# Optimization experiments

Measured on AMD Instinct MI355X. Metric: run time of the kernel, lower is better.

## Reference

```python
import jax, jax.numpy as jnp
import numpy as np

N_PER_G = 18
GRAPHS = 4096
N = GRAPHS * N_PER_G            # 73728 nodes
E = GRAPHS * N_PER_G * (N_PER_G - 1)  # 1253376 edges (fully connected per graph)
F_IN = 1536                     # sfreq * timestep
EPS = 1e-5
SLOPE = 0.01


def _lrelu(v):
    return jnp.where(v >= 0, v, SLOPE * v)


def setup_inputs() -> dict:
    key = jax.random.key(0)
    ks = jax.random.split(key, 32)
    # node features
    x = jax.random.normal(ks[0], (N, F_IN), dtype=jnp.float32)
    # fully-connected edges within each 18-node graph
    src, dst = np.meshgrid(np.arange(N_PER_G), np.arange(N_PER_G), indexing='ij')
    m = src != dst
    src, dst = src[m], dst[m]                      # [306]
    offs = (np.arange(GRAPHS) * N_PER_G)[:, None]
    row = (offs + src[None, :]).reshape(-1)
    col = (offs + dst[None, :]).reshape(-1)
    edge_index = jnp.asarray(np.stack([row, col]), dtype=jnp.int32)  # [2,E]
    edge_weight = jax.random.uniform(ks[1], (E,), dtype=jnp.float32)
    batch = jnp.asarray(np.arange(N) // N_PER_G, dtype=jnp.int32)

    def lin(k, fi, fo):
        kw, kb = jax.random.split(k)
        s = 1.0 / np.sqrt(fi)
        W = jax.random.uniform(kw, (fi, fo), jnp.float32, -s, s)
        b = jax.random.uniform(kb, (fo,), jnp.float32, -s, s)
        return W, b

    def bn(k, f):
        k1, k2 = jax.random.split(k)
        g = jnp.ones((f,), jnp.float32)
        be = jnp.zeros((f,), jnp.float32)
        rm = jax.random.normal(k1, (f,), jnp.float32) * 0.1
        rv = jax.random.uniform(k2, (f,), jnp.float32) + 0.5
        return g, be, rm, rv

    W1, b1 = lin(ks[2], F_IN, 32)
    W2, b2 = lin(ks[3], 32, 64)
    W3, b3 = lin(ks[4], 64, 128)
    g1, be1, rm1, rv1 = bn(ks[5], 32)
    g2, be2, rm2, rv2 = bn(ks[6], 64)
    g3, be3, rm3, rv3 = bn(ks[7], 128)
    fW1, fb1 = lin(ks[8], 128, 64)
    fW2, fb2 = lin(ks[9], 64, 32)
    fW3, fb3 = lin(ks[10], 32, 16)
    fW4, fb4 = lin(ks[11], 16, 1)

    return dict(x=x, edge_index=edge_index, edge_weight=edge_weight, batch=batch,
                W1=W1, b1=b1, g1=g1, be1=be1, rm1=rm1, rv1=rv1,
                W2=W2, b2=b2, g2=g2, be2=be2, rm2=rm2, rv2=rv2,
                W3=W3, b3=b3, g3=g3, be3=be3, rm3=rm3, rv3=rv3,
                fW1=fW1, fb1=fb1, fW2=fW2, fb2=fb2,
                fW3=fW3, fb3=fb3, fW4=fW4, fb4=fb4)


def _gcn_norm(edge_index, edge_weight):
    # add self loops (weight 1), symmetric normalization (PyG GCNConv, improved=False)
    row = jnp.concatenate([edge_index[0], jnp.arange(N, dtype=edge_index.dtype)])
    col = jnp.concatenate([edge_index[1], jnp.arange(N, dtype=edge_index.dtype)])
    w = jnp.concatenate([edge_weight, jnp.ones((N,), edge_weight.dtype)])
    deg = jax.ops.segment_sum(w, col, num_segments=N)
    dinv = jnp.where(deg > 0, jax.lax.rsqrt(jnp.maximum(deg, 1e-30)), 0.0)
    norm = dinv[row] * w * dinv[col]
    return row, col, norm


def _gcn(x, W, b, row, col, norm):
    h = x @ W                                       # [N, Fout]
    out = jax.ops.segment_sum(norm[:, None] * h[row], col, num_segments=N)
    return out + b


def _bn(h, g, be, rm, rv):
    return (h - rm) * jax.lax.rsqrt(rv + EPS) * g + be


def reference(x, edge_index, edge_weight, batch,
              W1, b1, g1, be1, rm1, rv1,
              W2, b2, g2, be2, rm2, rv2,
              W3, b3, g3, be3, rm3, rv3,
              fW1, fb1, fW2, fb2, fW3, fb3, fW4, fb4):
    row, col, norm = _gcn_norm(edge_index, edge_weight)
    h = _lrelu(_bn(_gcn(x, W1, b1, row, col, norm), g1, be1, rm1, rv1))
    h = _lrelu(_bn(_gcn(h, W2, b2, row, col, norm), g2, be2, rm2, rv2))
    h = _lrelu(_bn(_gcn(h, W3, b3, row, col, norm), g3, be3, rm3, rv3))
    # global mean pool over graphs
    sums = jax.ops.segment_sum(h, batch, num_segments=GRAPHS)
    cnt = jax.ops.segment_sum(jnp.ones((N,), h.dtype), batch, num_segments=GRAPHS)
    h = sums / jnp.maximum(cnt, 1.0)[:, None]       # [G,128]
    # MLP head (dropout = identity in eval)
    h = _lrelu(h @ fW1 + fb1)
    h = _lrelu(h @ fW2 + fb2)
    h = _lrelu(h @ fW3 + fb3)
    h = h @ fW4 + fb4
    return h.squeeze(-1)                            # [G]
```

## Files before the change

kernel.cpp:

```cpp
#include <hip/hip_runtime.h>
#include <stdint.h>

#define GRAPHS 4096
#define NPG 18
#define EPERG 306
#define FIN 1536
#define BN_EPS 1e-5f
#define SLOPE 0.01f

using short8  = __attribute__((ext_vector_type(8))) short;
using ushort8 = __attribute__((ext_vector_type(8))) unsigned short;
using f32x4   = __attribute__((ext_vector_type(4))) float;

__device__ __forceinline__ unsigned short f2bf(float f) {
  unsigned u = __builtin_bit_cast(unsigned, f);
  u += 0x7fffu + ((u >> 16) & 1u);
  return (unsigned short)(u >> 16);
}

__global__ void prep_kernel(const float* __restrict__ W1,
    const float* __restrict__ b1, const float* __restrict__ g1,
    const float* __restrict__ be1, const float* __restrict__ rm1, const float* __restrict__ rv1,
    const float* __restrict__ b2, const float* __restrict__ g2,
    const float* __restrict__ be2, const float* __restrict__ rm2, const float* __restrict__ rv2,
    const float* __restrict__ b3, const float* __restrict__ g3,
    const float* __restrict__ be3, const float* __restrict__ rm3, const float* __restrict__ rv3,
    unsigned short* __restrict__ w1frag, float* __restrict__ ab) {
  const int tid = threadIdx.x;
  if (blockIdx.x < 24) {
    int slot = blockIdx.x * 256 + tid;
    int L  = slot & 63;
    int nt = (slot >> 6) & 1;
    int ks = slot >> 7;
    int n  = nt * 16 + (L & 15);
    int kb = ks * 32 + ((L >> 4) << 3);
    ushort8 v;
#pragma unroll
    for (int j = 0; j < 8; ++j) v[j] = f2bf(W1[(kb + j) * 32 + n]);
    *((ushort8*)w1frag + slot) = v;
  } else {
    if (tid < 32) {
      float a = g1[tid] * rsqrtf(rv1[tid] + BN_EPS);
      ab[tid] = a; ab[32 + tid] = (b1[tid] - rm1[tid]) * a + be1[tid];
    }
    if (tid < 64) {
      float a = g2[tid] * rsqrtf(rv2[tid] + BN_EPS);
      ab[64 + tid] = a; ab[128 + tid] = (b2[tid] - rm2[tid]) * a + be2[tid];
    }
    if (tid < 128) {
      float a = g3[tid] * rsqrtf(rv3[tid] + BN_EPS);
      ab[192 + tid] = a; ab[320 + tid] = (b3[tid] - rm3[tid]) * a + be3[tid];
    }
  }
}

__global__ __launch_bounds__(256, 4) void gcn_main(
    const float* __restrict__ x, const float* __restrict__ ew,
    const float* __restrict__ W2, const float* __restrict__ W3,
    const float* __restrict__ fW1, const float* __restrict__ fb1,
    const float* __restrict__ fW2, const float* __restrict__ fb2,
    const float* __restrict__ fW3, const float* __restrict__ fb3,
    const float* __restrict__ fW4, const float* __restrict__ fb4,
    const unsigned short* __restrict__ w1frag, const float* __restrict__ ab,
    float* __restrict__ out) {
  const int g    = blockIdx.x;
  const int tid  = threadIdx.x;
  const int lane = tid & 63;
  const int wv   = tid >> 6;

  __shared__ float ew_s[EPERG];
  __shared__ float dinv_s[NPG];
  __shared__ float An[NPG][NPG + 1];
  __shared__ short xA[32][136];
  __shared__ float Pb[NPG][129];
  __shared__ float Hb[NPG][129];
  __shared__ float pooled[128];
  __shared__ float m1[64];
  __shared__ float m2[32];
  __shared__ float m3[16];

  for (int i = tid; i < EPERG; i += 256) ew_s[i] = ew[g * EPERG + i];
  for (int i = tid; i < 14 * 68; i += 256) {
    int r = 18 + i / 68, c = i % 68;
    ((int*)&xA[r][0])[c] = 0;
  }
  __syncthreads();

  if (tid < NPG) {
    float deg = 1.0f;
#pragma unroll
    for (int j = 0; j < 17; ++j) {
      int s = j + (j >= tid);
      deg += ew_s[s * 17 + (tid - (tid > s ? 1 : 0))];
    }
    dinv_s[tid] = rsqrtf(deg);
  }
  __syncthreads();

  for (int o = tid; o < NPG * NPG; o += 256) {
    int d = o / NPG, s = o - d * NPG;
    float v;
    if (d == s) v = dinv_s[d] * dinv_s[d];
    else        v = dinv_s[s] * ew_s[s * 17 + (d - (d > s ? 1 : 0))] * dinv_s[d];
    An[d][s] = v;
  }

  const int Mt = wv & 1, Nt = wv >> 1;
  const int arow  = Mt * 16 + (lane & 15);
  const int akoff = (lane >> 4) << 3;
  f32x4 acc = {0.f, 0.f, 0.f, 0.f};
  const float4* __restrict__ x4 = (const float4*)x + (size_t)g * 18 * 384;

  for (int c = 0; c < 12; ++c) {
    const int k0d4 = c * 32;
    for (int idx = tid; idx < 576; idx += 256) {
      int r = idx >> 5, c4 = idx & 31;
      float4 v = x4[r * 384 + k0d4 + c4];
      ushort4 b;
      b.x = f2bf(v.x); b.y = f2bf(v.y); b.z = f2bf(v.z); b.w = f2bf(v.w);
      *(ushort4*)(&xA[r][c4 * 4]) = b;
    }
    __syncthreads();
#pragma unroll
    for (int kk = 0; kk < 4; ++kk) {
      short8 af = *(const short8*)(&xA[arow][kk * 32 + akoff]);
      short8 bf = *(const short8*)(w1frag + (size_t)(((c * 4 + kk) * 2 + Nt) * 64 + lane) * 8);
      acc = __builtin_amdgcn_mfma_f32_16x16x32_bf16(af, bf, acc, 0, 0, 0);
    }
    __syncthreads();
  }

  {
    int ccol  = Nt * 16 + (lane & 15);
    int rbase = Mt * 16 + ((lane >> 4) << 2);
#pragma unroll
    for (int q = 0; q < 4; ++q) {
      int rr = rbase + q;
      if (rr < NPG) Pb[rr][ccol] = acc[q];
    }
  }
  __syncthreads();

  for (int o = tid; o < NPG * 32; o += 256) {
    int d = o >> 5, cc = o & 31;
    float s = 0.f;
#pragma unroll
    for (int ss = 0; ss < NPG; ++ss) s = fmaf(An[d][ss], Pb[ss][cc], s);
    float v = fmaf(s, ab[cc], ab[32 + cc]);
    Hb[d][cc] = v >= 0.f ? v : SLOPE * v;
  }
  __syncthreads();

  for (int o = tid; o < NPG * 64; o += 256) {
    int r = o >> 6, cc = o & 63;
    float s = 0.f;
#pragma unroll
    for (int k = 0; k < 32; ++k) s = fmaf(Hb[r][k], W2[k * 64 + cc], s);
    Pb[r][cc] = s;
  }
  __syncthreads();
  for (int o = tid; o < NPG * 64; o += 256) {
    int d = o >> 6, cc = o & 63;
    float s = 0.f;
#pragma unroll
    for (int ss = 0; ss < NPG; ++ss) s = fmaf(An[d][ss], Pb[ss][cc], s);
    float v = fmaf(s, ab[64 + cc], ab[128 + cc]);
    Hb[d][cc] = v >= 0.f ? v : SLOPE * v;
  }
  __syncthreads();

  for (int o = tid; o < NPG * 128; o += 256) {
    int r = o >> 7, cc = o & 127;
    float s = 0.f;
#pragma unroll
    for (int k = 0; k < 64; ++k) s = fmaf(Hb[r][k], W3[k * 128 + cc], s);
    Pb[r][cc] = s;
  }
  __syncthreads();
  for (int o = tid; o < NPG * 128; o += 256) {
    int d = o >> 7, cc = o & 127;
    float s = 0.f;
#pragma unroll
    for (int ss = 0; ss < NPG; ++ss) s = fmaf(An[d][ss], Pb[ss][cc], s);
    float v = fmaf(s, ab[192 + cc], ab[320 + cc]);
    Hb[d][cc] = v >= 0.f ? v : SLOPE * v;
  }
  __syncthreads();

  if (tid < 128) {
    float s = 0.f;
#pragma unroll
    for (int d = 0; d < NPG; ++d) s += Hb[d][tid];
    pooled[tid] = s * (1.0f / 18.0f);
  }
  __syncthreads();
  if (tid < 64) {
    float s = fb1[tid];
#pragma unroll 8
    for (int k = 0; k < 128; ++k) s = fmaf(pooled[k], fW1[k * 64 + tid], s);
    m1[tid] = s >= 0.f ? s : SLOPE * s;
  }
  __syncthreads();
  if (tid < 32) {
    float s = fb2[tid];
#pragma unroll
    for (int k = 0; k < 64; ++k) s = fmaf(m1[k], fW2[k * 32 + tid], s);
    m2[tid] = s >= 0.f ? s : SLOPE * s;
  }
  __syncthreads();
  if (tid < 16) {
    float s = fb3[tid];
#pragma unroll
    for (int k = 0; k < 32; ++k) s = fmaf(m2[k], fW3[k * 16 + tid], s);
    m3[tid] = s >= 0.f ? s : SLOPE * s;
  }
  __syncthreads();
  if (tid == 0) {
    float s = fb4[0];
#pragma unroll
    for (int k = 0; k < 16; ++k) s = fmaf(m3[k], fW4[k], s);
    out[g] = s;
  }
}

extern "C" void kernel_launch(void* const* d_in, const int* in_sizes, int n_in,
                              void* d_out, int out_size, void* d_ws, size_t ws_size,
                              hipStream_t stream) {
  const float* x   = (const float*)d_in[0];
  const float* ew  = (const float*)d_in[2];
  const float* W1  = (const float*)d_in[4];
  const float* b1  = (const float*)d_in[5];
  const float* g1  = (const float*)d_in[6];
  const float* be1 = (const float*)d_in[7];
  const float* rm1 = (const float*)d_in[8];
  const float* rv1 = (const float*)d_in[9];
  const float* W2  = (const float*)d_in[10];
  const float* b2  = (const float*)d_in[11];
  const float* g2  = (const float*)d_in[12];
  const float* be2 = (const float*)d_in[13];
  const float* rm2 = (const float*)d_in[14];
  const float* rv2 = (const float*)d_in[15];
  const float* W3  = (const float*)d_in[16];
  const float* b3  = (const float*)d_in[17];
  const float* g3  = (const float*)d_in[18];
  const float* be3 = (const float*)d_in[19];
  const float* rm3 = (const float*)d_in[20];
  const float* rv3 = (const float*)d_in[21];
  const float* fW1 = (const float*)d_in[22];
  const float* fb1 = (const float*)d_in[23];
  const float* fW2 = (const float*)d_in[24];
  const float* fb2 = (const float*)d_in[25];
  const float* fW3 = (const float*)d_in[26];
  const float* fb3 = (const float*)d_in[27];
  const float* fW4 = (const float*)d_in[28];
  const float* fb4 = (const float*)d_in[29];

  unsigned short* w1frag = (unsigned short*)d_ws;
  float* ab = (float*)((char*)d_ws + 98304);

  prep_kernel<<<25, 256, 0, stream>>>(W1, b1, g1, be1, rm1, rv1,
                                      b2, g2, be2, rm2, rv2,
                                      b3, g3, be3, rm3, rv3, w1frag, ab);
  gcn_main<<<GRAPHS, 256, 0, stream>>>(x, ew, W2, W3, fW1, fb1, fW2, fb2,
                                       fW3, fb3, fW4, fb4, w1frag, ab,
                                       (float*)d_out);
}
```

Baseline: 730.5 us.

## Split layer-1 GEMM into a flat MFMA kernel and reorder GCN aggregation

The per-graph layer-1 GEMM, which staged x through shared memory with a barrier per chunk, becomes a separate streaming kernel. It reads x rows directly into registers, converts them to bf16 and issues MFMAs over 16-row tiles, writing the projected features to a workspace buffer. The remaining kernel reads those features and reorders layers 2 and 3 so aggregation runs before the weight multiply, which shrinks aggregation width. The dense layers use pre-transposed weights with float4 dot products. This costs an extra launch and a global round trip for the intermediate buffer, in exchange for removing shared-memory staging and barriers from the memory-bound part.

```diff
diff --git a/kernel.cpp b/kernel.cpp
--- a/kernel.cpp
+++ b/kernel.cpp
@@ -25,7 +25,10 @@
     const float* __restrict__ be2, const float* __restrict__ rm2, const float* __restrict__ rv2,
     const float* __restrict__ b3, const float* __restrict__ g3,
     const float* __restrict__ be3, const float* __restrict__ rm3, const float* __restrict__ rv3,
-    unsigned short* __restrict__ w1frag, float* __restrict__ ab) {
+    const float* __restrict__ W2, const float* __restrict__ W3,
+    const float* __restrict__ fW1,
+    unsigned short* __restrict__ w1frag, float* __restrict__ ab,
+    float* __restrict__ W2t, float* __restrict__ W3t, float* __restrict__ fW1t) {
   const int tid = threadIdx.x;
   if (blockIdx.x < 24) {
     int slot = blockIdx.x * 256 + tid;
@@ -38,7 +41,7 @@
 #pragma unroll
     for (int j = 0; j < 8; ++j) v[j] = f2bf(W1[(kb + j) * 32 + n]);
     *((ushort8*)w1frag + slot) = v;
-  } else {
+  } else if (blockIdx.x == 24) {
     if (tid < 32) {
       float a = g1[tid] * rsqrtf(rv1[tid] + BN_EPS);
       ab[tid] = a; ab[32 + tid] = (b1[tid] - rm1[tid]) * a + be1[tid];
@@ -51,39 +54,85 @@
       float a = g3[tid] * rsqrtf(rv3[tid] + BN_EPS);
       ab[192 + tid] = a; ab[320 + tid] = (b3[tid] - rm3[tid]) * a + be3[tid];
     }
-  }
-}
-
-__global__ __launch_bounds__(256, 4) void gcn_main(
-    const float* __restrict__ x, const float* __restrict__ ew,
-    const float* __restrict__ W2, const float* __restrict__ W3,
-    const float* __restrict__ fW1, const float* __restrict__ fb1,
+  } else if (blockIdx.x == 25) {
+    for (int i = tid; i < 64 * 32; i += 256) {
+      int cc = i >> 5, k = i & 31;
+      W2t[i] = W2[k * 64 + cc];
+    }
+  } else if (blockIdx.x == 26) {
+    for (int i = tid; i < 128 * 64; i += 256) {
+      int cc = i >> 6, k = i & 63;
+      W3t[i] = W3[k * 128 + cc];
+    }
+  } else {
+    for (int i = tid; i < 64 * 128; i += 256) {
+      int cc = i >> 7, k = i & 127;
+      fW1t[i] = fW1[k * 64 + cc];
+    }
+  }
+}
+
+__global__ __launch_bounds__(128, 4) void l1_gemm(
+    const float* __restrict__ x, const unsigned short* __restrict__ w1frag,
+    float* __restrict__ p1) {
+  const int lane = threadIdx.x & 63;
+  const int wv   = threadIdx.x >> 6;
+  const int mt   = blockIdx.x * 2 + wv;
+  const int row  = mt * 16 + (lane & 15);
+  const float* __restrict__ xr = x + (size_t)row * FIN + ((lane >> 4) << 3);
+  const short8* __restrict__ wf = (const short8*)w1frag + lane;
+
+  f32x4 acc0 = {0.f, 0.f, 0.f, 0.f};
+  f32x4 acc1 = {0.f, 0.f, 0.f, 0.f};
+
+#pragma unroll 4
+  for (int ks = 0; ks < 48; ++ks) {
+    float4 a0 = *(const float4*)(xr + ks * 32);
+    float4 a1 = *(const float4*)(xr + ks * 32 + 4);
+    short8 af;
+    af[0] = (short)f2bf(a0.x); af[1] = (short)f2bf(a0.y);
+    af[2] = (short)f2bf(a0.z); af[3] = (short)f2bf(a0.w);
+    af[4] = (short)f2bf(a1.x); af[5] = (short)f2bf(a1.y);
+    af[6] = (short)f2bf(a1.z); af[7] = (short)f2bf(a1.w);
+    short8 b0 = wf[(ks * 2 + 0) * 64];
+    short8 b1 = wf[(ks * 2 + 1) * 64];
+    acc0 = __builtin_amdgcn_mfma_f32_16x16x32_bf16(af, b0, acc0, 0, 0, 0);
+    acc1 = __builtin_amdgcn_mfma_f32_16x16x32_bf16(af, b1, acc1, 0, 0, 0);
+  }
+
+  const int crow = mt * 16 + ((lane >> 4) << 2);
+  const int ccol = lane & 15;
+  float* p = p1 + (size_t)crow * 32 + ccol;
+#pragma unroll
+  for (int q = 0; q < 4; ++q) {
+    p[q * 32]      = acc0[q];
+    p[q * 32 + 16] = acc1[q];
+  }
+}
+
+__global__ __launch_bounds__(256, 4) void gcn_rest(
+    const float* __restrict__ ew, const float* __restrict__ p1,
+    const float* __restrict__ W2t, const float* __restrict__ W3t,
+    const float* __restrict__ fW1t, const float* __restrict__ fb1,
     const float* __restrict__ fW2, const float* __restrict__ fb2,
     const float* __restrict__ fW3, const float* __restrict__ fb3,
     const float* __restrict__ fW4, const float* __restrict__ fb4,
-    const unsigned short* __restrict__ w1frag, const float* __restrict__ ab,
-    float* __restrict__ out) {
-  const int g    = blockIdx.x;
-  const int tid  = threadIdx.x;
-  const int lane = tid & 63;
-  const int wv   = tid >> 6;
+    const float* __restrict__ ab, float* __restrict__ out) {
+  const int g   = blockIdx.x;
+  const int tid = threadIdx.x;
 
   __shared__ float ew_s[EPERG];
   __shared__ float dinv_s[NPG];
   __shared__ float An[NPG][NPG + 1];
-  __shared__ short xA[32][136];
-  __shared__ float Pb[NPG][129];
-  __shared__ float Hb[NPG][129];
-  __shared__ float pooled[128];
+  __shared__ __align__(16) float Pb[NPG][132];
+  __shared__ __align__(16) float Hb[NPG][132];
+  __shared__ __align__(16) float pooled[128];
   __shared__ float m1[64];
   __shared__ float m2[32];
   __shared__ float m3[16];
 
   for (int i = tid; i < EPERG; i += 256) ew_s[i] = ew[g * EPERG + i];
-  for (int i = tid; i < 14 * 68; i += 256) {
-    int r = 18 + i / 68, c = i % 68;
-    ((int*)&xA[r][0])[c] = 0;
-  }
+  for (int i = tid; i < NPG * 32; i += 256) Pb[i >> 5][i & 31] = p1[g * 576 + i];
   __syncthreads();
 
   if (tid < NPG) {
@@ -104,41 +153,6 @@
     else        v = dinv_s[s] * ew_s[s * 17 + (d - (d > s ? 1 : 0))] * dinv_s[d];
     An[d][s] = v;
   }
-
-  const int Mt = wv & 1, Nt = wv >> 1;
-  const int arow  = Mt * 16 + (lane & 15);
-  const int akoff = (lane >> 4) << 3;
-  f32x4 acc = {0.f, 0.f, 0.f, 0.f};
-  const float4* __restrict__ x4 = (const float4*)x + (size_t)g * 18 * 384;
-
-  for (int c = 0; c < 12; ++c) {
-    const int k0d4 = c * 32;
-    for (int idx = tid; idx < 576; idx += 256) {
-      int r = idx >> 5, c4 = idx & 31;
-      float4 v = x4[r * 384 + k0d4 + c4];
-      ushort4 b;
-      b.x = f2bf(v.x); b.y = f2bf(v.y); b.z = f2bf(v.z); b.w = f2bf(v.w);
-      *(ushort4*)(&xA[r][c4 * 4]) = b;
-    }
-    __syncthreads();
-#pragma unroll
-    for (int kk = 0; kk < 4; ++kk) {
-      short8 af = *(const short8*)(&xA[arow][kk * 32 + akoff]);
-      short8 bf = *(const short8*)(w1frag + (size_t)(((c * 4 + kk) * 2 + Nt) * 64 + lane) * 8);
-      acc = __builtin_amdgcn_mfma_f32_16x16x32_bf16(af, bf, acc, 0, 0, 0);
-    }
-    __syncthreads();
-  }
-
-  {
-    int ccol  = Nt * 16 + (lane & 15);
-    int rbase = Mt * 16 + ((lane >> 4) << 2);
-#pragma unroll
-    for (int q = 0; q < 4; ++q) {
-      int rr = rbase + q;
-      if (rr < NPG) Pb[rr][ccol] = acc[q];
-    }
-  }
   __syncthreads();
 
   for (int o = tid; o < NPG * 32; o += 256) {
@@ -151,39 +165,53 @@
   }
   __syncthreads();
 
+  for (int o = tid; o < NPG * 32; o += 256) {
+    int d = o >> 5, cc = o & 31;
+    float s = 0.f;
+#pragma unroll
+    for (int ss = 0; ss < NPG; ++ss) s = fmaf(An[d][ss], Hb[ss][cc], s);
+    Pb[d][cc] = s;
+  }
+  __syncthreads();
+
   for (int o = tid; o < NPG * 64; o += 256) {
     int r = o >> 6, cc = o & 63;
-    float s = 0.f;
-#pragma unroll
-    for (int k = 0; k < 32; ++k) s = fmaf(Hb[r][k], W2[k * 64 + cc], s);
-    Pb[r][cc] = s;
-  }
-  __syncthreads();
+    const float4* gp = (const float4*)(&Pb[r][0]);
+    const float4* wp = (const float4*)(W2t + cc * 32);
+    float s = 0.f;
+#pragma unroll
+    for (int k4 = 0; k4 < 8; ++k4) {
+      float4 a = gp[k4], b = wp[k4];
+      s = fmaf(a.x, b.x, s); s = fmaf(a.y, b.y, s);
+      s = fmaf(a.z, b.z, s); s = fmaf(a.w, b.w, s);
+    }
+    float v = fmaf(s, ab[64 + cc], ab[128 + cc]);
+    Hb[r][cc] = v >= 0.f ? v : SLOPE * v;
+  }
+  __syncthreads();
+
   for (int o = tid; o < NPG * 64; o += 256) {
     int d = o >> 6, cc = o & 63;
     float s = 0.f;
 #pragma unroll
-    for (int ss = 0; ss < NPG; ++ss) s = fmaf(An[d][ss], Pb[ss][cc], s);
-    float v = fmaf(s, ab[64 + cc], ab[128 + cc]);
-    Hb[d][cc] = v >= 0.f ? v : SLOPE * v;
+    for (int ss = 0; ss < NPG; ++ss) s = fmaf(An[d][ss], Hb[ss][cc], s);
+    Pb[d][cc] = s;
   }
   __syncthreads();
 
   for (int o = tid; o < NPG * 128; o += 256) {
     int r = o >> 7, cc = o & 127;
-    float s = 0.f;
-#pragma unroll
-    for (int k = 0; k < 64; ++k) s = fmaf(Hb[r][k], W3[k * 128 + cc], s);
-    Pb[r][cc] = s;
-  }
-  __syncthreads();
-  for (int o = tid; o < NPG * 128; o += 256) {
-    int d = o >> 7, cc = o & 127;
-    float s = 0.f;
-#pragma unroll
-    for (int ss = 0; ss < NPG; ++ss) s = fmaf(An[d][ss], Pb[ss][cc], s);
+    const float4* gp = (const float4*)(&Pb[r][0]);
+    const float4* wp = (const float4*)(W3t + cc * 64);
+    float s = 0.f;
+#pragma unroll
+    for (int k4 = 0; k4 < 16; ++k4) {
+      float4 a = gp[k4], b = wp[k4];
+      s = fmaf(a.x, b.x, s); s = fmaf(a.y, b.y, s);
+      s = fmaf(a.z, b.z, s); s = fmaf(a.w, b.w, s);
+    }
     float v = fmaf(s, ab[192 + cc], ab[320 + cc]);
-    Hb[d][cc] = v >= 0.f ? v : SLOPE * v;
+    Hb[r][cc] = v >= 0.f ? v : SLOPE * v;
   }
   __syncthreads();
 
@@ -195,9 +223,15 @@
   }
   __syncthreads();
   if (tid < 64) {
+    const float4* pp = (const float4*)pooled;
+    const float4* wp = (const float4*)(fW1t + tid * 128);
     float s = fb1[tid];
-#pragma unroll 8
-    for (int k = 0; k < 128; ++k) s = fmaf(pooled[k], fW1[k * 64 + tid], s);
+#pragma unroll
+    for (int k4 = 0; k4 < 32; ++k4) {
+      float4 a = pp[k4], b = wp[k4];
+      s = fmaf(a.x, b.x, s); s = fmaf(a.y, b.y, s);
+      s = fmaf(a.z, b.z, s); s = fmaf(a.w, b.w, s);
+    }
     m1[tid] = s >= 0.f ? s : SLOPE * s;
   }
   __syncthreads();
@@ -256,12 +290,18 @@
   const float* fb4 = (const float*)d_in[29];
 
   unsigned short* w1frag = (unsigned short*)d_ws;
-  float* ab = (float*)((char*)d_ws + 98304);
-
-  prep_kernel<<<25, 256, 0, stream>>>(W1, b1, g1, be1, rm1, rv1,
+  float* ab   = (float*)((char*)d_ws + 98304);
+  float* W2t  = (float*)((char*)d_ws + 100352);
+  float* W3t  = (float*)((char*)d_ws + 108544);
+  float* fW1t = (float*)((char*)d_ws + 141312);
+  float* p1   = (float*)((char*)d_ws + 174080);
+
+  prep_kernel<<<28, 256, 0, stream>>>(W1, b1, g1, be1, rm1, rv1,
                                       b2, g2, be2, rm2, rv2,
-                                      b3, g3, be3, rm3, rv3, w1frag, ab);
-  gcn_main<<<GRAPHS, 256, 0, stream>>>(x, ew, W2, W3, fW1, fb1, fW2, fb2,
-                                       fW3, fb3, fW4, fb4, w1frag, ab,
-                                       (float*)d_out);
-}
+                                      b3, g3, be3, rm3, rv3,
+                                      W2, W3, fW1,
+                                      w1frag, ab, W2t, W3t, fW1t);
+  l1_gemm<<<2304, 128, 0, stream>>>(x, w1frag, p1);
+  gcn_rest<<<GRAPHS, 256, 0, stream>>>(ew, p1, W2t, W3t, fW1t, fb1, fW2, fb2,
+                                       fW3, fb3, fW4, fb4, ab, (float*)d_out);
+}
```

Result: slower. 747.0 us (+2.3%).

## Batch eight graphs per block with register-fed MFMA and per-wave GCN layers

Applied to the files above, without the earlier changes.

Each block now handles eight graphs. The first-layer projection reads x directly from global memory into bf16 MFMA fragments, with no LDS staging or per-chunk barriers. Later layers and the MLP head run per wave with only waitcnt fences, and aggregation is reordered to come before the small dense projections. The grid shrinks to 512 blocks, which lowers parallelism and raises register pressure (large wc arrays).

```diff
diff --git a/kernel.cpp b/kernel.cpp
--- a/kernel.cpp
+++ b/kernel.cpp
@@ -7,6 +7,9 @@
 #define FIN 1536
 #define BN_EPS 1e-5f
 #define SLOPE 0.01f
+#define GPB 8
+#define RPB 144
+#define NTILE 9
 
 using short8  = __attribute__((ext_vector_type(8))) short;
 using ushort8 = __attribute__((ext_vector_type(8))) unsigned short;
@@ -16,6 +19,19 @@
   unsigned u = __builtin_bit_cast(unsigned, f);
   u += 0x7fffu + ((u >> 16) & 1u);
   return (unsigned short)(u >> 16);
+}
+
+__device__ __forceinline__ short8 pack_bf16(const float4& a0, const float4& a1) {
+  short8 af;
+  af[0] = (short)f2bf(a0.x); af[1] = (short)f2bf(a0.y);
+  af[2] = (short)f2bf(a0.z); af[3] = (short)f2bf(a0.w);
+  af[4] = (short)f2bf(a1.x); af[5] = (short)f2bf(a1.y);
+  af[6] = (short)f2bf(a1.z); af[7] = (short)f2bf(a1.w);
+  return af;
+}
+
+__device__ __forceinline__ void wave_fence() {
+  asm volatile("s_waitcnt lgkmcnt(0)" ::: "memory");
 }
 
 __global__ void prep_kernel(const float* __restrict__ W1,
@@ -54,172 +70,196 @@
   }
 }
 
-__global__ __launch_bounds__(256, 4) void gcn_main(
+__global__ __launch_bounds__(256, 2) void gcn_fused(
     const float* __restrict__ x, const float* __restrict__ ew,
+    const unsigned short* __restrict__ w1frag, const float* __restrict__ ab,
     const float* __restrict__ W2, const float* __restrict__ W3,
     const float* __restrict__ fW1, const float* __restrict__ fb1,
     const float* __restrict__ fW2, const float* __restrict__ fb2,
     const float* __restrict__ fW3, const float* __restrict__ fb3,
     const float* __restrict__ fW4, const float* __restrict__ fb4,
-    const unsigned short* __restrict__ w1frag, const float* __restrict__ ab,
     float* __restrict__ out) {
-  const int g    = blockIdx.x;
+  const int bid  = blockIdx.x;
   const int tid  = threadIdx.x;
   const int lane = tid & 63;
   const int wv   = tid >> 6;
 
-  __shared__ float ew_s[EPERG];
-  __shared__ float dinv_s[NPG];
-  __shared__ float An[NPG][NPG + 1];
-  __shared__ short xA[32][136];
-  __shared__ float Pb[NPG][129];
-  __shared__ float Hb[NPG][129];
-  __shared__ float pooled[128];
-  __shared__ float m1[64];
-  __shared__ float m2[32];
-  __shared__ float m3[16];
-
-  for (int i = tid; i < EPERG; i += 256) ew_s[i] = ew[g * EPERG + i];
-  for (int i = tid; i < 14 * 68; i += 256) {
-    int r = 18 + i / 68, c = i % 68;
-    ((int*)&xA[r][0])[c] = 0;
+  __shared__ __align__(16) float P1[RPB][36];
+  __shared__ float ew_s[GPB * EPERG];
+  __shared__ float dinv_s[GPB][NPG];
+  __shared__ float An_s[GPB][NPG][19];
+  __shared__ __align__(16) float BufA[4][NPG][68];
+  __shared__ __align__(16) float BufB[4][NPG][68];
+
+  for (int i = tid; i < GPB * EPERG; i += 256)
+    ew_s[i] = ew[(size_t)bid * (GPB * EPERG) + i];
+
+  const int arow = lane & 15;
+  const int akg  = lane >> 4;
+  const short8* __restrict__ wf = (const short8*)w1frag + lane;
+  const float* __restrict__ xg = x + (size_t)bid * RPB * FIN;
+
+  for (int t = wv; t < NTILE; t += 4) {
+    f32x4 acc0 = {0.f, 0.f, 0.f, 0.f};
+    f32x4 acc1 = {0.f, 0.f, 0.f, 0.f};
+    const float* __restrict__ xr = xg + (size_t)(t * 16 + arow) * FIN + (akg << 3);
+#pragma unroll 4
+    for (int ks = 0; ks < 48; ++ks) {
+      float4 a0 = *(const float4*)(xr + ks * 32);
+      float4 a1 = *(const float4*)(xr + ks * 32 + 4);
+      short8 af = pack_bf16(a0, a1);
+      acc0 = __builtin_amdgcn_mfma_f32_16x16x32_bf16(af, wf[(ks * 2 + 0) * 64], acc0, 0, 0, 0);
+      acc1 = __builtin_amdgcn_mfma_f32_16x16x32_bf16(af, wf[(ks * 2 + 1) * 64], acc1, 0, 0, 0);
+    }
+    const int crow = t * 16 + (akg << 2);
+#pragma unroll
+    for (int q = 0; q < 4; ++q) {
+      P1[crow + q][arow]      = acc0[q];
+      P1[crow + q][arow + 16] = acc1[q];
+    }
   }
   __syncthreads();
 
-  if (tid < NPG) {
+  if (tid < GPB * NPG) {
+    int j = tid / NPG, d = tid - j * NPG;
+    const float* e = ew_s + j * EPERG;
     float deg = 1.0f;
 #pragma unroll
-    for (int j = 0; j < 17; ++j) {
-      int s = j + (j >= tid);
-      deg += ew_s[s * 17 + (tid - (tid > s ? 1 : 0))];
-    }
-    dinv_s[tid] = rsqrtf(deg);
+    for (int k = 0; k < 17; ++k) {
+      int s = k + (k >= d);
+      deg += e[s * 17 + (d - (d > s ? 1 : 0))];
+    }
+    dinv_s[j][d] = rsqrtf(deg);
   }
   __syncthreads();
 
-  for (int o = tid; o < NPG * NPG; o += 256) {
-    int d = o / NPG, s = o - d * NPG;
+  for (int o = tid; o < GPB * NPG * NPG; o += 256) {
+    int j = o / (NPG * NPG), rm = o - j * (NPG * NPG);
+    int d = rm / NPG, s = rm - d * NPG;
     float v;
-    if (d == s) v = dinv_s[d] * dinv_s[d];
-    else        v = dinv_s[s] * ew_s[s * 17 + (d - (d > s ? 1 : 0))] * dinv_s[d];
-    An[d][s] = v;
-  }
-
-  const int Mt = wv & 1, Nt = wv >> 1;
-  const int arow  = Mt * 16 + (lane & 15);
-  const int akoff = (lane >> 4) << 3;
-  f32x4 acc = {0.f, 0.f, 0.f, 0.f};
-  const float4* __restrict__ x4 = (const float4*)x + (size_t)g * 18 * 384;
-
-  for (int c = 0; c < 12; ++c) {
-    const int k0d4 = c * 32;
-    for (int idx = tid; idx < 576; idx += 256) {
-      int r = idx >> 5, c4 = idx & 31;
-      float4 v = x4[r * 384 + k0d4 + c4];
-      ushort4 b;
-      b.x = f2bf(v.x); b.y = f2bf(v.y); b.z = f2bf(v.z); b.w = f2bf(v.w);
-      *(ushort4*)(&xA[r][c4 * 4]) = b;
-    }
-    __syncthreads();
-#pragma unroll
-    for (int kk = 0; kk < 4; ++kk) {
-      short8 af = *(const short8*)(&xA[arow][kk * 32 + akoff]);
-      short8 bf = *(const short8*)(w1frag + (size_t)(((c * 4 + kk) * 2 + Nt) * 64 + lane) * 8);
-      acc = __builtin_amdgcn_mfma_f32_16x16x32_bf16(af, bf, acc, 0, 0, 0);
-    }
-    __syncthreads();
-  }
-
-  {
-    int ccol  = Nt * 16 + (lane & 15);
-    int rbase = Mt * 16 + ((lane >> 4) << 2);
-#pragma unroll
-    for (int q = 0; q < 4; ++q) {
-      int rr = rbase + q;
-      if (rr < NPG) Pb[rr][ccol] = acc[q];
-    }
+    if (d == s) v = dinv_s[j][d] * dinv_s[j][d];
+    else        v = dinv_s[j][s] * ew_s[j * EPERG + s * 17 + (d - (d > s ? 1 : 0))] * dinv_s[j][d];
+    An_s[j][d][s] = v;
   }
   __syncthreads();
 
-  for (int o = tid; o < NPG * 32; o += 256) {
-    int d = o >> 5, cc = o & 31;
-    float s = 0.f;
-#pragma unroll
-    for (int ss = 0; ss < NPG; ++ss) s = fmaf(An[d][ss], Pb[ss][cc], s);
-    float v = fmaf(s, ab[cc], ab[32 + cc]);
-    Hb[d][cc] = v >= 0.f ? v : SLOPE * v;
-  }
-  __syncthreads();
-
-  for (int o = tid; o < NPG * 64; o += 256) {
-    int r = o >> 6, cc = o & 63;
-    float s = 0.f;
-#pragma unroll
-    for (int k = 0; k < 32; ++k) s = fmaf(Hb[r][k], W2[k * 64 + cc], s);
-    Pb[r][cc] = s;
-  }
-  __syncthreads();
-  for (int o = tid; o < NPG * 64; o += 256) {
-    int d = o >> 6, cc = o & 63;
-    float s = 0.f;
-#pragma unroll
-    for (int ss = 0; ss < NPG; ++ss) s = fmaf(An[d][ss], Pb[ss][cc], s);
-    float v = fmaf(s, ab[64 + cc], ab[128 + cc]);
-    Hb[d][cc] = v >= 0.f ? v : SLOPE * v;
-  }
-  __syncthreads();
-
-  for (int o = tid; o < NPG * 128; o += 256) {
-    int r = o >> 7, cc = o & 127;
-    float s = 0.f;
-#pragma unroll
-    for (int k = 0; k < 64; ++k) s = fmaf(Hb[r][k], W3[k * 128 + cc], s);
-    Pb[r][cc] = s;
-  }
-  __syncthreads();
-  for (int o = tid; o < NPG * 128; o += 256) {
-    int d = o >> 7, cc = o & 127;
-    float s = 0.f;
-#pragma unroll
-    for (int ss = 0; ss < NPG; ++ss) s = fmaf(An[d][ss], Pb[ss][cc], s);
-    float v = fmaf(s, ab[192 + cc], ab[320 + cc]);
-    Hb[d][cc] = v >= 0.f ? v : SLOPE * v;
-  }
-  __syncthreads();
-
-  if (tid < 128) {
-    float s = 0.f;
-#pragma unroll
-    for (int d = 0; d < NPG; ++d) s += Hb[d][tid];
-    pooled[tid] = s * (1.0f / 18.0f);
-  }
-  __syncthreads();
-  if (tid < 64) {
-    float s = fb1[tid];
-#pragma unroll 8
-    for (int k = 0; k < 128; ++k) s = fmaf(pooled[k], fW1[k * 64 + tid], s);
-    m1[tid] = s >= 0.f ? s : SLOPE * s;
-  }
-  __syncthreads();
-  if (tid < 32) {
-    float s = fb2[tid];
-#pragma unroll
-    for (int k = 0; k < 64; ++k) s = fmaf(m1[k], fW2[k * 32 + tid], s);
-    m2[tid] = s >= 0.f ? s : SLOPE * s;
-  }
-  __syncthreads();
-  if (tid < 16) {
-    float s = fb3[tid];
-#pragma unroll
-    for (int k = 0; k < 32; ++k) s = fmaf(m2[k], fW3[k * 16 + tid], s);
-    m3[tid] = s >= 0.f ? s : SLOPE * s;
-  }
-  __syncthreads();
-  if (tid == 0) {
-    float s = fb4[0];
-#pragma unroll
-    for (int k = 0; k < 16; ++k) s = fmaf(m3[k], fW4[k], s);
-    out[g] = s;
+  float (*A_)[68] = BufA[wv];
+  float (*B_)[68] = BufB[wv];
+
+#pragma unroll 1
+  for (int jj = 0; jj < 2; ++jj) {
+    const int j = wv + (jj << 2);
+    const float (*An)[19] = An_s[j];
+    const float* P1g = &P1[j * NPG][0];
+
+    for (int o4 = lane; o4 < 144; o4 += 64) {
+      int d = o4 >> 3, cb = (o4 & 7) << 2;
+      f32x4 s = {0.f, 0.f, 0.f, 0.f};
+#pragma unroll
+      for (int ss = 0; ss < NPG; ++ss) {
+        float a = An[d][ss];
+        f32x4 p = *(const f32x4*)(P1g + ss * 36 + cb);
+        s[0] = fmaf(a, p[0], s[0]); s[1] = fmaf(a, p[1], s[1]);
+        s[2] = fmaf(a, p[2], s[2]); s[3] = fmaf(a, p[3], s[3]);
+      }
+      f32x4 al = *(const f32x4*)(ab + cb), be = *(const f32x4*)(ab + 32 + cb);
+#pragma unroll
+      for (int q = 0; q < 4; ++q) {
+        float v = fmaf(s[q], al[q], be[q]);
+        s[q] = v >= 0.f ? v : SLOPE * v;
+      }
+      *(f32x4*)&A_[d][cb] = s;
+    }
+    wave_fence();
+
+    for (int o4 = lane; o4 < 144; o4 += 64) {
+      int d = o4 >> 3, cb = (o4 & 7) << 2;
+      f32x4 s = {0.f, 0.f, 0.f, 0.f};
+#pragma unroll
+      for (int ss = 0; ss < NPG; ++ss) {
+        float a = An[d][ss];
+        f32x4 p = *(const f32x4*)&A_[ss][cb];
+        s[0] = fmaf(a, p[0], s[0]); s[1] = fmaf(a, p[1], s[1]);
+        s[2] = fmaf(a, p[2], s[2]); s[3] = fmaf(a, p[3], s[3]);
+      }
+      *(f32x4*)&B_[d][cb] = s;
+    }
+    wave_fence();
+
+    {
+      float wc[32];
+#pragma unroll
+      for (int k = 0; k < 32; ++k) wc[k] = W2[k * 64 + lane];
+      const float al = ab[64 + lane], be = ab[128 + lane];
+      for (int r2 = 0; r2 < NPG; ++r2) {
+        float s = 0.f;
+#pragma unroll
+        for (int k4 = 0; k4 < 8; ++k4) {
+          f32x4 g = *(const f32x4*)&B_[r2][k4 * 4];
+          s = fmaf(g[0], wc[k4 * 4 + 0], s); s = fmaf(g[1], wc[k4 * 4 + 1], s);
+          s = fmaf(g[2], wc[k4 * 4 + 2], s); s = fmaf(g[3], wc[k4 * 4 + 3], s);
+        }
+        float v = fmaf(s, al, be);
+        A_[r2][lane] = v >= 0.f ? v : SLOPE * v;
+      }
+    }
+    wave_fence();
+
+    for (int o4 = lane; o4 < 288; o4 += 64) {
+      int d = o4 >> 4, cb = (o4 & 15) << 2;
+      f32x4 s = {0.f, 0.f, 0.f, 0.f};
+#pragma unroll
+      for (int ss = 0; ss < NPG; ++ss) {
+        float a = An[d][ss];
+        f32x4 p = *(const f32x4*)&A_[ss][cb];
+        s[0] = fmaf(a, p[0], s[0]); s[1] = fmaf(a, p[1], s[1]);
+        s[2] = fmaf(a, p[2], s[2]); s[3] = fmaf(a, p[3], s[3]);
+      }
+      *(f32x4*)&B_[d][cb] = s;
+    }
+    wave_fence();
+
+    float pool0 = 0.f, pool1 = 0.f;
+#pragma unroll
+    for (int h = 0; h < 2; ++h) {
+      const int cc = (h << 6) + lane;
+      float wc[64];
+#pragma unroll
+      for (int k = 0; k < 64; ++k) wc[k] = W3[k * 128 + cc];
+      const float al = ab[192 + cc], be = ab[320 + cc];
+      float pr = 0.f;
+      for (int r3 = 0; r3 < NPG; ++r3) {
+        float s = 0.f;
+#pragma unroll
+        for (int k4 = 0; k4 < 16; ++k4) {
+          f32x4 g = *(const f32x4*)&B_[r3][k4 * 4];
+          s = fmaf(g[0], wc[k4 * 4 + 0], s); s = fmaf(g[1], wc[k4 * 4 + 1], s);
+          s = fmaf(g[2], wc[k4 * 4 + 2], s); s = fmaf(g[3], wc[k4 * 4 + 3], s);
+        }
+        float v = fmaf(s, al, be);
+        pr += (v >= 0.f ? v : SLOPE * v);
+      }
+      if (h == 0) pool0 = pr * (1.0f / 18.0f); else pool1 = pr * (1.0f / 18.0f);
+    }
+
+    float s1 = fb1[lane];
+#pragma unroll
+    for (int k = 0; k < 64; ++k) s1 = fmaf(__shfl(pool0, k), fW1[k * 64 + lane], s1);
+#pragma unroll
+    for (int k = 0; k < 64; ++k) s1 = fmaf(__shfl(pool1, k), fW1[(64 + k) * 64 + lane], s1);
+    s1 = s1 >= 0.f ? s1 : SLOPE * s1;
+    float s2 = fb2[lane & 31];
+#pragma unroll
+    for (int k = 0; k < 64; ++k) s2 = fmaf(__shfl(s1, k), fW2[k * 32 + (lane & 31)], s2);
+    s2 = s2 >= 0.f ? s2 : SLOPE * s2;
+    float s3 = fb3[lane & 15];
+#pragma unroll
+    for (int k = 0; k < 32; ++k) s3 = fmaf(__shfl(s2, k), fW3[k * 16 + (lane & 15)], s3);
+    s3 = s3 >= 0.f ? s3 : SLOPE * s3;
+    float s4 = fb4[0];
+#pragma unroll
+    for (int k = 0; k < 16; ++k) s4 = fmaf(__shfl(s3, k), fW4[k], s4);
+    if (lane == 0) out[(bid << 3) + j] = s4;
   }
 }
 
@@ -256,12 +296,13 @@
   const float* fb4 = (const float*)d_in[29];
 
   unsigned short* w1frag = (unsigned short*)d_ws;
-  float* ab = (float*)((char*)d_ws + 98304);
+  float* ab   = (float*)((char*)d_ws + 98304);
 
   prep_kernel<<<25, 256, 0, stream>>>(W1, b1, g1, be1, rm1, rv1,
                                       b2, g2, be2, rm2, rv2,
-                                      b3, g3, be3, rm3, rv3, w1frag, ab);
-  gcn_main<<<GRAPHS, 256, 0, stream>>>(x, ew, W2, W3, fW1, fb1, fW2, fb2,
-                                       fW3, fb3, fW4, fb4, w1frag, ab,
-                                       (float*)d_out);
-}
+                                      b3, g3, be3, rm3, rv3,
+                                      w1frag, ab);
+  gcn_fused<<<512, 256, 0, stream>>>(x, ew, w1frag, ab, W2, W3, fW1,
+                                     fb1, fW2, fb2, fW3, fb3, fW4, fb4,
+                                     (float*)d_out);
+}
```

After: 1.013 ms. +38.7%, slower.
